# Optimization experiments

Measured on AMD Instinct MI355X. Metric: run time of the kernel, lower is better.

## Reference

```python
import jax, jax.numpy as jnp
import numpy as np

B, S, H = 2, 1024, 1024
NH, HD = 16, 64
W = 4  # attention_window / number of cached previous-layer states
LS_INIT = 0.1  # layer_scale_init_value
EPS = 1e-5


def _layernorm(x, scale, bias):
    mu = jnp.mean(x, axis=-1, keepdims=True)
    var = jnp.mean(jnp.square(x - mu), axis=-1, keepdims=True)
    return (x - mu) * jax.lax.rsqrt(var + EPS) * scale + bias


def _rope(x, pos):
    # x: [B, L, NH, HD], pos: [L]
    half = x.shape[-1] // 2
    freq = 1.0 / (10000.0 ** (jnp.arange(half, dtype=x.dtype) / half))
    ang = pos.astype(x.dtype)[:, None] * freq[None, :]           # [L, half]
    cos = jnp.cos(ang)[None, :, None, :]
    sin = jnp.sin(ang)[None, :, None, :]
    x1, x2 = jnp.split(x, 2, axis=-1)
    return jnp.concatenate([x1 * cos - x2 * sin, x1 * sin + x2 * cos], axis=-1)


def setup_inputs() -> dict:
    key = jax.random.key(0)
    ks = jax.random.split(key, 8)
    w_std = 0.02
    return {
        'hidden_states': jax.random.normal(ks[0], (B, S, H), jnp.float32),
        'cache_states': jax.random.normal(ks[1], (W, B, S, H), jnp.float32),
        'ln_scale': jnp.ones((H,), jnp.float32),
        'ln_bias': jnp.zeros((H,), jnp.float32),
        'Wq': jax.random.normal(ks[2], (H, NH * HD), jnp.float32) * w_std,
        'Wk': jax.random.normal(ks[3], (H, NH * HD), jnp.float32) * w_std,
        'Wv': jax.random.normal(ks[4], (H, NH * HD), jnp.float32) * w_std,
        'Wo': jax.random.normal(ks[5], (NH * HD, H), jnp.float32) * w_std,
        'gate_param': jax.random.normal(ks[6], (H,), jnp.float32),
        'layer_scale_param': jnp.full((H,), LS_INIT, jnp.float32),
    }


def reference(hidden_states, cache_states, ln_scale, ln_bias, Wq, Wk, Wv, Wo,
              gate_param, layer_scale_param):
    b, s, h = hidden_states.shape
    w = cache_states.shape[0]

    # pre-norm
    normed = _layernorm(hidden_states, ln_scale, ln_bias)

    # gather cached previous-layer states (already normalized in cache) and
    # stack them with the current layer along the KV axis: [B, (W+1)*S, H]
    prev_flat = jnp.transpose(cache_states, (1, 0, 2, 3)).reshape(b, w * s, h)
    kv_in = jnp.concatenate([prev_flat, normed], axis=1)

    q = (normed @ Wq).reshape(b, s, NH, HD)
    k = (kv_in @ Wk).reshape(b, (w + 1) * s, NH, HD)
    v = (kv_in @ Wv).reshape(b, (w + 1) * s, NH, HD)

    pos_q = jnp.arange(s)
    pos_k = jnp.tile(jnp.arange(s), w + 1)  # same token positions per layer
    q = _rope(q, pos_q)
    k = _rope(k, pos_k)

    scale = 1.0 / jnp.sqrt(jnp.asarray(HD, hidden_states.dtype))
    scores = jnp.einsum('bqhd,bkhd->bhqk', q, k) * scale   # [B,NH,S,(W+1)S]
    attn = jax.nn.softmax(scores, axis=-1)
    ctx = jnp.einsum('bhqk,bkhd->bqhd', attn, v).reshape(b, s, NH * HD)
    attn_out = ctx @ Wo

    # gated residual with layer scale; cross_layer = most recent cached state
    cross_layer = cache_states[-1]
    g = jax.nn.sigmoid(gate_param)
    combined = g * attn_out + (1.0 - g) * cross_layer
    output = hidden_states + layer_scale_param * combined

    # LRU cache update: evict oldest slot, append normalized new state
    new_state = _layernorm(output, ln_scale, ln_bias)
    new_cache = jnp.concatenate([cache_states[1:], new_state[None]], axis=0)
    return output, new_cache
```

## Files before the change

### kernel.cpp

```cpp
#include <hip/hip_runtime.h>
#include <math.h>

typedef unsigned short u16;

constexpr int cB = 2;
constexpr int cS = 1024;
constexpr int cH = 1024;
constexpr int cNH = 16;
constexpr int cHD = 64;
constexpr int cW = 4;
constexpr int cL = (cW + 1) * cS;
constexpr float cEPS = 1e-5f;

typedef short s16x8 __attribute__((ext_vector_type(8)));
typedef float f32x4 __attribute__((ext_vector_type(4)));

__device__ __forceinline__ float u2f(u16 u) {
  union { unsigned int i; float f; } x; x.i = ((unsigned int)u) << 16; return x.f;
}
__device__ __forceinline__ u16 f2u(float f) {
  union { float f; unsigned int i; } x; x.f = f;
  unsigned int i = x.i;
  i += 0x7fffu + ((i >> 16) & 1u);
  return (u16)(i >> 16);
}
__device__ __forceinline__ u16 f2u_rt(float f) {
  union { __bf16 b; u16 u; } c; c.b = (__bf16)f; return c.u;
}
__device__ __forceinline__ s16x8 ld_frag(const u16* p) {
  uint4 v = *(const uint4*)p;
  union { uint4 u; s16x8 s; } c; c.u = v; return c.s;
}
__device__ __forceinline__ s16x8 u4_frag(uint4 v) {
  union { uint4 u; s16x8 s; } c; c.u = v; return c.s;
}
__device__ __forceinline__ void gl_lds16(const u16* g, u16* l) {
  __builtin_amdgcn_global_load_lds(
      (const __attribute__((address_space(1))) unsigned int*)g,
      (__attribute__((address_space(3))) unsigned int*)l, 16, 0, 0);
}
template <int CTRL>
__device__ __forceinline__ float dpp_fmax(float x) {
  union { float f; int i; } a, r;
  a.f = x;
  r.i = __builtin_amdgcn_update_dpp(a.i, a.i, CTRL, 0xF, 0xF, true);
  return fmaxf(x, r.f);
}

__global__ __launch_bounds__(256) void ln_f32(
    const float* __restrict__ src, float* __restrict__ dst,
    const float* __restrict__ scale, const float* __restrict__ bias)
{
  int r = blockIdx.x;
  int t = threadIdx.x;
  const float* sp = src + (size_t)r * cH;
  float4 x = ((const float4*)sp)[t];
  float s1 = x.x + x.y + x.z + x.w;
  float s2 = x.x * x.x + x.y * x.y + x.z * x.z + x.w * x.w;
  #pragma unroll
  for (int off = 32; off > 0; off >>= 1) {
    s1 += __shfl_down(s1, off);
    s2 += __shfl_down(s2, off);
  }
  __shared__ float w1[4], w2[4];
  __shared__ float stat[2];
  int wid = t >> 6, lid = t & 63;
  if (lid == 0) { w1[wid] = s1; w2[wid] = s2; }
  __syncthreads();
  if (t == 0) {
    float a = w1[0] + w1[1] + w1[2] + w1[3];
    float b = w2[0] + w2[1] + w2[2] + w2[3];
    float mu = a * (1.f / cH);
    float var = b * (1.f / cH) - mu * mu;
    if (var < 0.f) var = 0.f;
    stat[0] = mu; stat[1] = rsqrtf(var + cEPS);
  }
  __syncthreads();
  float mu = stat[0], rs = stat[1];
  int h0 = t * 4;
  float4 sc = *(const float4*)(scale + h0);
  float4 bi = *(const float4*)(bias + h0);
  float4 o;
  o.x = (x.x - mu) * rs * sc.x + bi.x;
  o.y = (x.y - mu) * rs * sc.y + bi.y;
  o.z = (x.z - mu) * rs * sc.z + bi.z;
  o.w = (x.w - mu) * rs * sc.w + bi.w;
  *(float4*)(dst + (size_t)r * cH + h0) = o;
}

__global__ __launch_bounds__(256) void prep(
    const float* __restrict__ W0, const float* __restrict__ W1,
    const float* __restrict__ W2, const float* __restrict__ W3,
    u16* __restrict__ Wt,
    const float* __restrict__ cache, u16* __restrict__ kvin,
    const float* __restrict__ hidden,
    const float* __restrict__ scale, const float* __restrict__ bias)
{
  __shared__ float tile[32][33];
  __shared__ float red[10];
  int t = threadIdx.x;
  int bid = blockIdx.x;
  if (bid < 4096) {
    int mat = bid >> 10;
    int k0 = ((bid >> 5) & 31) * 32, n0 = (bid & 31) * 32;
    const float* W = (mat == 0) ? W0 : (mat == 1) ? W1 : (mat == 2) ? W2 : W3;
    u16* out = Wt + (size_t)mat * cH * cH;
    int r = t >> 3, c = (t & 7) * 4;
    float4 v = *(const float4*)(W + (size_t)(k0 + r) * cH + n0 + c);
    tile[r][c] = v.x; tile[r][c + 1] = v.y; tile[r][c + 2] = v.z; tile[r][c + 3] = v.w;
    __syncthreads();
    ushort4 o; u16* op = (u16*)&o;
    #pragma unroll
    for (int j = 0; j < 4; j++) op[j] = f2u(tile[c + j][r]);
    *(ushort4*)(out + (size_t)(n0 + r) * cH + k0 + c) = o;
  } else if (bid < 12288) {
    int blk = bid - 4096;
    int b = blk >> 12, w = (blk >> 10) & 3, s = blk & 1023;
    const float* src = cache + ((size_t)((w * cB + b) * cS + s)) * cH;
    u16* dst = kvin + ((size_t)(b * cL + w * cS + s)) * cH;
    float4 v = *(const float4*)(src + t * 4);
    ushort4 o; u16* op = (u16*)&o;
    op[0] = f2u(v.x); op[1] = f2u(v.y); op[2] = f2u(v.z); op[3] = f2u(v.w);
    *(ushort4*)(dst + t * 4) = o;
  } else {
    int r = bid - 12288;
    const float* sp = hidden + (size_t)r * cH;
    float4 x = ((const float4*)sp)[t];
    float s1 = x.x + x.y + x.z + x.w;
    float s2 = x.x * x.x + x.y * x.y + x.z * x.z + x.w * x.w;
    #pragma unroll
    for (int off = 32; off > 0; off >>= 1) {
      s1 += __shfl_down(s1, off);
      s2 += __shfl_down(s2, off);
    }
    int wid = t >> 6, lid = t & 63;
    if (lid == 0) { red[wid] = s1; red[4 + wid] = s2; }
    __syncthreads();
    if (t == 0) {
      float a = red[0] + red[1] + red[2] + red[3];
      float b2 = red[4] + red[5] + red[6] + red[7];
      float mu = a * (1.f / cH);
      float var = b2 * (1.f / cH) - mu * mu;
      if (var < 0.f) var = 0.f;
      red[8] = mu; red[9] = rsqrtf(var + cEPS);
    }
    __syncthreads();
    float mu = red[8], rs = red[9];
    int h0 = t * 4;
    float4 sc = *(const float4*)(scale + h0);
    float4 bi = *(const float4*)(bias + h0);
    int b = r >> 10, s = r & (cS - 1);
    u16* dp = kvin + ((size_t)(b * cL + cW * cS + s)) * cH + h0;
    ushort4 o; u16* op = (u16*)&o;
    op[0] = f2u((x.x - mu) * rs * sc.x + bi.x);
    op[1] = f2u((x.y - mu) * rs * sc.y + bi.y);
    op[2] = f2u((x.z - mu) * rs * sc.z + bi.z);
    op[3] = f2u((x.w - mu) * rs * sc.w + bi.w);
    *(ushort4*)dp = o;
  }
}

constexpr int GBM = 128, GBN = 128, TLD = 136;

__global__ __launch_bounds__(256) void mgemm(
    const u16* __restrict__ A, const u16* __restrict__ Wt,
    int a_rpb, int a_base, int a_stride,
    int c_rpb, int mode,
    u16* __restrict__ Cb, u16* __restrict__ Cb2,
    const float* __restrict__ hidden, const float* __restrict__ cachefull,
    const float* __restrict__ gate, const float* __restrict__ lsc,
    float* __restrict__ outp)
{
  __shared__ __align__(16) u16 smem[128 * TLD];

  int t = threadIdx.x;
  int m0 = blockIdx.y * GBM, n0 = blockIdx.x * GBN;
  int wave = t >> 6, lane = t & 63, l15 = lane & 15, quad = lane >> 4;
  int wm = (wave >> 1) * 64, wn = (wave & 1) * 64;

  int sr = t >> 2, sk = (t & 3) * 8;
  int rg0 = m0 + sr, rg1 = rg0 + 64;
  int ab0 = rg0 / a_rpb, ab1 = rg1 / a_rpb;
  const u16* arow0 = A + (size_t)(ab0 * a_stride + a_base + (rg0 - ab0 * a_rpb)) * cH + sk;
  const u16* arow1 = A + (size_t)(ab1 * a_stride + a_base + (rg1 - ab1 * a_rpb)) * cH + sk;
  const u16* wrow0 = Wt + (size_t)(n0 + sr) * cH + sk;
  const u16* wrow1 = Wt + (size_t)(n0 + sr + 64) * cH + sk;

  u16* As0 = smem;
  u16* Bs0 = smem + 8192;
  int wofs = wave * 512;

  f32x4 acc[4][4] = {};

  gl_lds16(arow0, As0 + wofs);
  gl_lds16(arow1, As0 + 2048 + wofs);
  gl_lds16(wrow0, Bs0 + wofs);
  gl_lds16(wrow1, Bs0 + 2048 + wofs);

  constexpr int NK = cH / 32;
  for (int kt = 0; kt < NK; kt++) {
    int cur = kt & 1;
    asm volatile("" ::: "memory");
    __builtin_amdgcn_s_barrier();
    asm volatile("" ::: "memory");
    int nk = kt + 1; if (nk == NK) nk = 0;
    int nko = nk * 32;
    u16* Abn = As0 + (cur ^ 1) * 4096;
    u16* Bbn = Bs0 + (cur ^ 1) * 4096;
    gl_lds16(arow0 + nko, Abn + wofs);
    gl_lds16(arow1 + nko, Abn + 2048 + wofs);
    gl_lds16(wrow0 + nko, Bbn + wofs);
    gl_lds16(wrow1 + nko, Bbn + 2048 + wofs);
    asm volatile("s_waitcnt vmcnt(4)" ::: "memory");
    __builtin_amdgcn_s_barrier();
    asm volatile("" ::: "memory");
    const u16* Ab = As0 + cur * 4096;
    const u16* Bb = Bs0 + cur * 4096;
    s16x8 af[4], bf[4];
    #pragma unroll
    for (int mt = 0; mt < 4; mt++)
      af[mt] = *(const s16x8*)&Ab[(wm + mt * 16 + l15) * 32 + quad * 8];
    #pragma unroll
    for (int nt = 0; nt < 4; nt++)
      bf[nt] = *(const s16x8*)&Bb[(wn + nt * 16 + l15) * 32 + quad * 8];
    #pragma unroll
    for (int mt = 0; mt < 4; mt++)
      #pragma unroll
      for (int nt = 0; nt < 4; nt++)
        acc[mt][nt] = __builtin_amdgcn_mfma_f32_16x16x32_bf16(af[mt], bf[nt], acc[mt][nt], 0, 0, 0);
  }

  int mode_eff = mode;
  u16* Cout = Cb;
  int nbase = n0;
  if (mode == 5) {
    if (n0 < cH) { mode_eff = 1; }
    else { mode_eff = 3; Cout = Cb2; nbase = n0 - cH; }
  }

  if (mode_eff == 1) {
    constexpr float RC = 13.287712379549449f / 32.f;
    float fr0 = exp2f(-(float)l15 * RC);
    float fr1 = exp2f(-(float)(l15 + 16) * RC);
    #pragma unroll
    for (int mt = 0; mt < 4; mt++)
      #pragma unroll
      for (int i = 0; i < 4; i++) {
        int rg = m0 + wm + mt * 16 + quad * 4 + i;
        int bo = rg / c_rpb, lo = rg - bo * c_rpb;
        int pos = lo & (cS - 1);
        float sn0, cs0, sn1, cs1;
        sincosf((float)pos * fr0, &sn0, &cs0);
        sincosf((float)pos * fr1, &sn1, &cs1);
        float v0 = acc[mt][0][i], v1 = acc[mt][1][i];
        float v2 = acc[mt][2][i], v3 = acc[mt][3][i];
        float rr[4];
        rr[0] = v0 * cs0 - v2 * sn0;
        rr[1] = v1 * cs1 - v3 * sn1;
        rr[2] = v0 * sn0 + v2 * cs0;
        rr[3] = v1 * sn1 + v3 * cs1;
        #pragma unroll
        for (int nt = 0; nt < 4; nt++) {
          int n = nbase + wn + nt * 16 + l15;
          int h = n >> 6, d = n & 63;
          Cout[(((size_t)(bo * cNH + h) * c_rpb + lo) * cHD) + d] = f2u(rr[nt]);
        }
      }
  } else if (mode_eff == 3) {
    u16* t2 = smem;
    asm volatile("s_waitcnt vmcnt(0)" ::: "memory");
    __syncthreads();
    #pragma unroll
    for (int mt = 0; mt < 4; mt++)
      #pragma unroll
      for (int nt = 0; nt < 4; nt++) {
        ushort4 o; u16* op = (u16*)&o;
        #pragma unroll
        for (int i = 0; i < 4; i++) op[i] = f2u(acc[mt][nt][i]);
        *(ushort4*)&t2[(size_t)(wn + nt * 16 + l15) * TLD + wm + mt * 16 + quad * 4] = o;
      }
    __syncthreads();
    int n_l = t >> 1, mh = (t & 1) * 64;
    int bo = m0 / c_rpb;
    int lo = m0 - bo * c_rpb + mh;
    int n = nbase + n_l, h = n >> 6, d = n & 63;
    u16* dst = Cout + ((size_t)(bo * cNH + h) * cHD + d) * (size_t)c_rpb + lo;
    #pragma unroll
    for (int j = 0; j < 8; j++)
      *(uint4*)(dst + j * 8) = *(const uint4*)&t2[(size_t)n_l * TLD + mh + j * 8];
  } else {
    float gv[4], lv[4];
    #pragma unroll
    for (int nt = 0; nt < 4; nt++) {
      int n = n0 + wn + nt * 16 + l15;
      gv[nt] = 1.f / (1.f + __expf(-gate[n]));
      lv[nt] = lsc[n];
    }
    #pragma unroll
    for (int mt = 0; mt < 4; mt++)
      #pragma unroll
      for (int i = 0; i < 4; i++) {
        int rg = m0 + wm + mt * 16 + quad * 4 + i;
        size_t rbase = (size_t)rg * cH;
        #pragma unroll
        for (int nt = 0; nt < 4; nt++) {
          int n = n0 + wn + nt * 16 + l15;
          float hid = hidden[rbase + n];
          float cr = cachefull[(size_t)3 * cB * cS * cH + rbase + n];
          outp[rbase + n] = hid + lv[nt] * (gv[nt] * acc[mt][nt][i] + (1.f - gv[nt]) * cr);
        }
      }
  }
}

constexpr int ACK = 64;
constexpr int PLD = 72;
constexpr int KSPLIT = 3;
constexpr int SPLT_T = 27;
constexpr int NRB = cB * cNH * cS;

__global__ __launch_bounds__(256, 3) void attn_mfma(
    const u16* __restrict__ Q, const u16* __restrict__ K, const u16* __restrict__ Vt,
    float* __restrict__ o0, float* __restrict__ o1, float* __restrict__ o2,
    float* __restrict__ mlbuf)
{
  __shared__ __align__(16) u16 kls[2][ACK * cHD];
  __shared__ u16 pbuf[4][2][16 * PLD];

  int t = threadIdx.x;
  int wave = t >> 6, lane = t & 63;
  int l15 = lane & 15, quad = lane >> 4;
  int qt = blockIdx.x, h = blockIdx.y;
  int bz = blockIdx.z;
  int b = bz & (cB - 1), split = bz >> 1;
  int q0a = qt * 128 + wave * 16;
  int q0b = q0a + 64;
  int kbase = split * SPLT_T * ACK;
  int NIT = (split == KSPLIT - 1) ? (cL / ACK - (KSPLIT - 1) * SPLT_T) : SPLT_T;

  const u16* qpa = Q + ((size_t)(b * cNH + h) * cS + q0a) * cHD;
  const u16* qpb = qpa + (size_t)64 * cHD;
  const char* kp = (const char*)(K + ((size_t)(b * cNH + h) * cL + kbase) * cHD);
  const u16* vp = Vt + (size_t)(b * cNH + h) * cHD * cL + kbase;
  u16* pwA = &pbuf[wave][0][0];
  u16* pwB = &pbuf[wave][1][0];

  int P0 = wave * 1024 + lane * 16;
  int P1 = P0 + 4096;
  int s0 = P0 ^ (((P0 >> 7) & 7) << 4);
  int s1 = P1 ^ (((P1 >> 7) & 7) << 4);
  int fsw0 = (quad * 16) ^ ((l15 & 7) << 4);
  int fsw1 = (64 + quad * 16) ^ ((l15 & 7) << 4);

  s16x8 qa0 = ld_frag(qpa + (size_t)l15 * cHD + quad * 8);
  s16x8 qa1 = ld_frag(qpa + (size_t)l15 * cHD + 32 + quad * 8);
  s16x8 qb0f = ld_frag(qpb + (size_t)l15 * cHD + quad * 8);
  s16x8 qb1f = ld_frag(qpb + (size_t)l15 * cHD + 32 + quad * 8);

  gl_lds16((const u16*)(kp + s0), (u16*)((char*)&kls[0][0] + wave * 1024));
  gl_lds16((const u16*)(kp + s1), (u16*)((char*)&kls[0][0] + 4096 + wave * 1024));

  f32x4 oacc[2][4] = {};
  float mrowA[4], lrowA[4], mrowB[4], lrowB[4];
  #pragma unroll
  for (int i = 0; i < 4; i++) {
    mrowA[i] = -1e30f; lrowA[i] = 0.f;
    mrowB[i] = -1e30f; lrowB[i] = 0.f;
  }

  constexpr float SCL = 0.125f * 1.4426950408889634f;

  for (int kt = 0; kt < NIT; kt++) {
    int cur = kt & 1;
    uint4 v01[4];
    #pragma unroll
    for (int dt = 0; dt < 2; dt++) {
      const u16* vr = vp + (size_t)(dt * 16 + l15) * cL + kt * ACK;
      v01[2 * dt]     = *(const uint4*)(vr + quad * 8);
      v01[2 * dt + 1] = *(const uint4*)(vr + 32 + quad * 8);
    }
    asm volatile("" ::: "memory");
    __builtin_amdgcn_s_barrier();
    asm volatile("" ::: "memory");
    int nk = kt + 1; if (nk == NIT) nk = 0;
    const char* kn = kp + (size_t)nk * (ACK * cHD * 2);
    gl_lds16((const u16*)(kn + s0), (u16*)((char*)&kls[cur ^ 1][0] + wave * 1024));
    gl_lds16((const u16*)(kn + s1), (u16*)((char*)&kls[cur ^ 1][0] + 4096 + wave * 1024));
    asm volatile("s_waitcnt vmcnt(6)" ::: "memory");
    __builtin_amdgcn_s_barrier();
    asm volatile("" ::: "memory");
    const char* kc = (const char*)&kls[cur][0];
    f32x4 scA[4], scB[4];
    __builtin_amdgcn_s_setprio(1);
    #pragma unroll
    for (int nt = 0; nt < 4; nt++) {
      s16x8 kf0 = *(const s16x8*)(kc + (nt * 16 + l15) * 128 + fsw0);
      s16x8 kf1 = *(const s16x8*)(kc + (nt * 16 + l15) * 128 + fsw1);
      f32x4 a = {};
      a = __builtin_amdgcn_mfma_f32_16x16x32_bf16(qa0, kf0, a, 0, 0, 0);
      a = __builtin_amdgcn_mfma_f32_16x16x32_bf16(qa1, kf1, a, 0, 0, 0);
      scA[nt] = a * SCL;
      f32x4 c = {};
      c = __builtin_amdgcn_mfma_f32_16x16x32_bf16(qb0f, kf0, c, 0, 0, 0);
      c = __builtin_amdgcn_mfma_f32_16x16x32_bf16(qb1f, kf1, c, 0, 0, 0);
      scB[nt] = c * SCL;
    }
    __builtin_amdgcn_s_setprio(0);
    float mxA[4], mxB[4];
    #pragma unroll
    for (int i = 0; i < 4; i++) {
      mxA[i] = fmaxf(fmaxf(scA[0][i], scA[1][i]), fmaxf(scA[2][i], scA[3][i]));
      mxB[i] = fmaxf(fmaxf(scB[0][i], scB[1][i]), fmaxf(scB[2][i], scB[3][i]));
    }
    #pragma unroll
    for (int i = 0; i < 4; i++) {
      mxA[i] = dpp_fmax<0xB1>(mxA[i]);  mxB[i] = dpp_fmax<0xB1>(mxB[i]);
      mxA[i] = dpp_fmax<0x4E>(mxA[i]);  mxB[i] = dpp_fmax<0x4E>(mxB[i]);
      mxA[i] = dpp_fmax<0x141>(mxA[i]); mxB[i] = dpp_fmax<0x141>(mxB[i]);
      mxA[i] = dpp_fmax<0x140>(mxA[i]); mxB[i] = dpp_fmax<0x140>(mxB[i]);
    }
    bool needA = (mxA[0] > mrowA[0]) | (mxA[1] > mrowA[1]) |
                 (mxA[2] > mrowA[2]) | (mxA[3] > mrowA[3]);
    if (__any(needA)) {
      float alpha[4];
      #pragma unroll
      for (int i = 0; i < 4; i++) {
        float mn = fmaxf(mrowA[i], mxA[i]);
        alpha[i] = exp2f(mrowA[i] - mn);
        mrowA[i] = mn;
        lrowA[i] *= alpha[i];
      }
      #pragma unroll
      for (int dt = 0; dt < 4; dt++)
        #pragma unroll
        for (int i = 0; i < 4; i++) oacc[0][dt][i] *= alpha[i];
    }
    bool needB = (mxB[0] > mrowB[0]) | (mxB[1] > mrowB[1]) |
                 (mxB[2] > mrowB[2]) | (mxB[3] > mrowB[3]);
    if (__any(needB)) {
      float alpha[4];
      #pragma unroll
      for (int i = 0; i < 4; i++) {
        float mn = fmaxf(mrowB[i], mxB[i]);
        alpha[i] = exp2f(mrowB[i] - mn);
        mrowB[i] = mn;
        lrowB[i] *= alpha[i];
      }
      #pragma unroll
      for (int dt = 0; dt < 4; dt++)
        #pragma unroll
        for (int i = 0; i < 4; i++) oacc[1][dt][i] *= alpha[i];
    }
    {
      float ps[4] = {};
      #pragma unroll
      for (int nt = 0; nt < 4; nt++)
        #pragma unroll
        for (int i = 0; i < 4; i++) {
          float p = exp2f(scA[nt][i] - mrowA[i]);
          ps[i] += p;
          pwA[(quad * 4 + i) * PLD + nt * 16 + l15] = f2u_rt(p);
        }
      #pragma unroll
      for (int i = 0; i < 4; i++) lrowA[i] += ps[i];
    }
    uint4 v23[4];
    #pragma unroll
    for (int dt = 2; dt < 4; dt++) {
      const u16* vr = vp + (size_t)(dt * 16 + l15) * cL + kt * ACK;
      v23[2 * (dt - 2)]     = *(const uint4*)(vr + quad * 8);
      v23[2 * (dt - 2) + 1] = *(const uint4*)(vr + 32 + quad * 8);
    }
    {
      float ps[4] = {};
      #pragma unroll
      for (int nt = 0; nt < 4; nt++)
        #pragma unroll
        for (int i = 0; i < 4; i++) {
          float p = exp2f(scB[nt][i] - mrowB[i]);
          ps[i] += p;
          pwB[(quad * 4 + i) * PLD + nt * 16 + l15] = f2u_rt(p);
        }
      #pragma unroll
      for (int i = 0; i < 4; i++) lrowB[i] += ps[i];
    }
    s16x8 pfA0 = *(const s16x8*)&pwA[l15 * PLD + quad * 8];
    s16x8 pfA1 = *(const s16x8*)&pwA[l15 * PLD + 32 + quad * 8];
    s16x8 pfB0 = *(const s16x8*)&pwB[l15 * PLD + quad * 8];
    s16x8 pfB1 = *(const s16x8*)&pwB[l15 * PLD + 32 + quad * 8];
    __builtin_amdgcn_s_setprio(1);
    #pragma unroll
    for (int dt = 0; dt < 2; dt++) {
      oacc[0][dt] = __builtin_amdgcn_mfma_f32_16x16x32_bf16(pfA0, u4_frag(v01[2 * dt]), oacc[0][dt], 0, 0, 0);
      oacc[0][dt] = __builtin_amdgcn_mfma_f32_16x16x32_bf16(pfA1, u4_frag(v01[2 * dt + 1]), oacc[0][dt], 0, 0, 0);
      oacc[1][dt] = __builtin_amdgcn_mfma_f32_16x16x32_bf16(pfB0, u4_frag(v01[2 * dt]), oacc[1][dt], 0, 0, 0);
      oacc[1][dt] = __builtin_amdgcn_mfma_f32_16x16x32_bf16(pfB1, u4_frag(v01[2 * dt + 1]), oacc[1][dt], 0, 0, 0);
    }
    #pragma unroll
    for (int dt = 2; dt < 4; dt++) {
      int vi = 2 * (dt - 2);
      oacc[0][dt] = __builtin_amdgcn_mfma_f32_16x16x32_bf16(pfA0, u4_frag(v23[vi]), oacc[0][dt], 0, 0, 0);
      oacc[0][dt] = __builtin_amdgcn_mfma_f32_16x16x32_bf16(pfA1, u4_frag(v23[vi + 1]), oacc[0][dt], 0, 0, 0);
      oacc[1][dt] = __builtin_amdgcn_mfma_f32_16x16x32_bf16(pfB0, u4_frag(v23[vi]), oacc[1][dt], 0, 0, 0);
      oacc[1][dt] = __builtin_amdgcn_mfma_f32_16x16x32_bf16(pfB1, u4_frag(v23[vi + 1]), oacc[1][dt], 0, 0, 0);
    }
    __builtin_amdgcn_s_setprio(0);
  }
  #pragma unroll
  for (int off = 1; off < 16; off <<= 1)
    #pragma unroll
    for (int i = 0; i < 4; i++) {
      lrowA[i] += __shfl_xor(lrowA[i], off);
      lrowB[i] += __shfl_xor(lrowB[i], off);
    }
  float* ob = (split == 0) ? o0 : (split == 1) ? o1 : o2;
  #pragma unroll
  for (int x = 0; x < 2; x++) {
    int qbase = x ? q0b : q0a;
    #pragma unroll
    for (int i = 0; i < 4; i++) {
      int q = qbase + quad * 4 + i;
      size_t Rl = (size_t)(b * cNH + h) * cS + q;
      float* orow = ob + Rl * cHD;
      #pragma unroll
      for (int dt = 0; dt < 4; dt++)
        orow[dt * 16 + l15] = oacc[x][dt][i];
      if (l15 == 0) {
        mlbuf[((size_t)split * NRB + Rl) * 2]     = x ? mrowB[i] : mrowA[i];
        mlbuf[((size_t)split * NRB + Rl) * 2 + 1] = x ? lrowB[i] : lrowA[i];
      }
    }
  }
}

__global__ __launch_bounds__(256) void attn_merge(
    const float* __restrict__ o0, const float* __restrict__ o1,
    const float* __restrict__ o2,
    const float* __restrict__ mlbuf, u16* __restrict__ ctx)
{
  int t = threadIdx.x;
  int R = blockIdx.x * 4 + (t >> 6);
  int d = t & 63;
  float ms[KSPLIT], ls[KSPLIT];
  float m = -1e30f;
  #pragma unroll
  for (int s = 0; s < KSPLIT; s++) {
    ms[s] = mlbuf[((size_t)s * NRB + R) * 2];
    ls[s] = mlbuf[((size_t)s * NRB + R) * 2 + 1];
    m = fmaxf(m, ms[s]);
  }
  const float* ops[KSPLIT] = {o0, o1, o2};
  float num = 0.f, den = 0.f;
  #pragma unroll
  for (int s = 0; s < KSPLIT; s++) {
    float a = exp2f(ms[s] - m);
    num += ops[s][(size_t)R * cHD + d] * a;
    den += ls[s] * a;
  }
  float val = num / den;
  int q = R & (cS - 1), h = (R >> 10) & 15, b = R >> 14;
  ctx[((size_t)b * cS + q) * cH + h * cHD + d] = f2u(val);
}

extern "C" void kernel_launch(void* const* d_in, const int* in_sizes, int n_in,
                              void* d_out, int out_size, void* d_ws, size_t ws_size,
                              hipStream_t stream)
{
  const float* hidden = (const float*)d_in[0];
  const float* cache  = (const float*)d_in[1];
  const float* ln_s   = (const float*)d_in[2];
  const float* ln_b   = (const float*)d_in[3];
  const float* Wq     = (const float*)d_in[4];
  const float* Wk     = (const float*)d_in[5];
  const float* Wv     = (const float*)d_in[6];
  const float* Wo     = (const float*)d_in[7];
  const float* gate   = (const float*)d_in[8];
  const float* lsc    = (const float*)d_in[9];
  float* outp = (float*)d_out;

  u16* kvin = (u16*)d_ws;
  u16* vt   = kvin + (size_t)cB * cL * cH;
  float* opart = (float*)(vt + (size_t)cB * cL * cH);
  float* o0 = opart;
  float* o1 = opart + (size_t)cB * cNH * cS * cHD;
  u16* qb  = kvin;
  u16* ctx = kvin + (size_t)2 * 1024 * 1024;
  float* o2 = (float*)(kvin + (size_t)4 * 1024 * 1024);
  float* mlbuf = (float*)(kvin + (size_t)8 * 1024 * 1024);
  u16* kb = (u16*)(outp + (size_t)cB * cS * cH);
  u16* Wt = (u16*)(outp + (size_t)(1 + 3) * cB * cS * cH);
  u16* Wt_q = Wt;
  u16* Wt_k = Wt + (size_t)cH * cH;
  u16* Wt_o = Wt + (size_t)3 * cH * cH;

  prep<<<14336, 256, 0, stream>>>(Wq, Wk, Wv, Wo, Wt, cache, kvin,
                                  hidden, ln_s, ln_b);

  mgemm<<<dim3(16, (cB * cL) / GBM), 256, 0, stream>>>(
      kvin, Wt_k, cL, 0, cL, cL, 5, kb, vt, nullptr, nullptr, nullptr, nullptr, nullptr);
  mgemm<<<dim3(8, (cB * cS) / GBM), 256, 0, stream>>>(
      kvin, Wt_q, cS, cW * cS, cL, cS, 1, qb, nullptr, nullptr, nullptr, nullptr, nullptr, nullptr);

  attn_mfma<<<dim3(cS / 128, cNH, cB * KSPLIT), 256, 0, stream>>>(
      qb, kb, vt, o0, o1, o2, mlbuf);
  attn_merge<<<(cB * cNH * cS) / 4, 256, 0, stream>>>(o0, o1, o2, mlbuf, ctx);

  mgemm<<<dim3(8, (cB * cS) / GBM), 256, 0, stream>>>(
      ctx, Wt_o, cB * cS, 0, cB * cS, cB * cS, 2, nullptr, nullptr,
      hidden, cache, gate, lsc, outp);

  hipMemcpyAsync(outp + (size_t)cB * cS * cH, cache + (size_t)cB * cS * cH,
                 (size_t)(cW - 1) * cB * cS * cH * sizeof(float),
                 hipMemcpyDeviceToDevice, stream);
  ln_f32<<<cB * cS, 256, 0, stream>>>(outp, outp + (size_t)cW * cB * cS * cH, ln_s, ln_b);
}
```

Measured before the change: 365.8 us.

## Merge Q and KV projection GEMMs into one launch; precompute RoPE table

```diff
diff --git a/kernel.cpp b/kernel.cpp
--- a/kernel.cpp
+++ b/kernel.cpp
@@ -94,7 +94,8 @@
     u16* __restrict__ Wt,
     const float* __restrict__ cache, u16* __restrict__ kvin,
     const float* __restrict__ hidden,
-    const float* __restrict__ scale, const float* __restrict__ bias)
+    const float* __restrict__ scale, const float* __restrict__ bias,
+    float2* __restrict__ ropetab)
 {
   __shared__ float tile[32][33];
   __shared__ float red[10];
@@ -122,7 +123,7 @@
     ushort4 o; u16* op = (u16*)&o;
     op[0] = f2u(v.x); op[1] = f2u(v.y); op[2] = f2u(v.z); op[3] = f2u(v.w);
     *(ushort4*)(dst + t * 4) = o;
-  } else {
+  } else if (bid < 14336) {
     int r = bid - 12288;
     const float* sp = hidden + (size_t)r * cH;
     float4 x = ((const float4*)sp)[t];
@@ -157,6 +158,14 @@
     op[2] = f2u((x.z - mu) * rs * sc.z + bi.z);
     op[3] = f2u((x.w - mu) * rs * sc.w + bi.w);
     *(ushort4*)dp = o;
+  } else {
+    int idx = (bid - 14336) * 256 + t;
+    int pos = idx >> 5, d = idx & 31;
+    constexpr float RC = 13.287712379549449f / 32.f;
+    float fr = exp2f(-(float)d * RC);
+    float sn, cs;
+    sincosf((float)pos * fr, &sn, &cs);
+    ropetab[idx] = make_float2(cs, sn);
   }
 }
 
@@ -166,7 +175,8 @@
     const u16* __restrict__ A, const u16* __restrict__ Wt,
     int a_rpb, int a_base, int a_stride,
     int c_rpb, int mode,
-    u16* __restrict__ Cb, u16* __restrict__ Cb2,
+    u16* __restrict__ Cb, u16* __restrict__ Cb2, u16* __restrict__ Cb3,
+    const float2* __restrict__ ropetab,
     const float* __restrict__ hidden, const float* __restrict__ cachefull,
     const float* __restrict__ gate, const float* __restrict__ lsc,
     float* __restrict__ outp)
@@ -174,7 +184,27 @@
   __shared__ __align__(16) u16 smem[128 * TLD];
 
   int t = threadIdx.x;
-  int m0 = blockIdx.y * GBM, n0 = blockIdx.x * GBN;
+  int bx = blockIdx.x, by = blockIdx.y;
+  int eff_mode = mode;
+  const u16* WtU = Wt;
+  u16* CbU = Cb; u16* Cb2U = Cb2;
+  if (mode == 6) {
+    if (bx < 1280) {
+      eff_mode = 5;
+      by = bx >> 4; bx = bx & 15;
+      a_rpb = cL; a_base = 0; a_stride = cL; c_rpb = cL;
+      WtU = Wt + (size_t)cH * cH;
+    } else {
+      eff_mode = 1;
+      int id = bx - 1280;
+      by = id >> 3; bx = id & 7;
+      a_rpb = cS; a_base = cW * cS; a_stride = cL; c_rpb = cS;
+      WtU = Wt;
+      CbU = Cb3;
+    }
+  }
+
+  int m0 = by * GBM, n0 = bx * GBN;
   int wave = t >> 6, lane = t & 63, l15 = lane & 15, quad = lane >> 4;
   int wm = (wave >> 1) * 64, wn = (wave & 1) * 64;
 
@@ -183,8 +213,8 @@
   int ab0 = rg0 / a_rpb, ab1 = rg1 / a_rpb;
   const u16* arow0 = A + (size_t)(ab0 * a_stride + a_base + (rg0 - ab0 * a_rpb)) * cH + sk;
   const u16* arow1 = A + (size_t)(ab1 * a_stride + a_base + (rg1 - ab1 * a_rpb)) * cH + sk;
-  const u16* wrow0 = Wt + (size_t)(n0 + sr) * cH + sk;
-  const u16* wrow1 = Wt + (size_t)(n0 + sr + 64) * cH + sk;
+  const u16* wrow0 = WtU + (size_t)(n0 + sr) * cH + sk;
+  const u16* wrow1 = WtU + (size_t)(n0 + sr + 64) * cH + sk;
 
   u16* As0 = smem;
   u16* Bs0 = smem + 8192;
@@ -230,18 +260,15 @@
         acc[mt][nt] = __builtin_amdgcn_mfma_f32_16x16x32_bf16(af[mt], bf[nt], acc[mt][nt], 0, 0, 0);
   }
 
-  int mode_eff = mode;
-  u16* Cout = Cb;
+  int mode_eff = eff_mode;
+  u16* Cout = CbU;
   int nbase = n0;
-  if (mode == 5) {
+  if (eff_mode == 5) {
     if (n0 < cH) { mode_eff = 1; }
-    else { mode_eff = 3; Cout = Cb2; nbase = n0 - cH; }
+    else { mode_eff = 3; Cout = Cb2U; nbase = n0 - cH; }
   }
 
   if (mode_eff == 1) {
-    constexpr float RC = 13.287712379549449f / 32.f;
-    float fr0 = exp2f(-(float)l15 * RC);
-    float fr1 = exp2f(-(float)(l15 + 16) * RC);
     #pragma unroll
     for (int mt = 0; mt < 4; mt++)
       #pragma unroll
@@ -249,16 +276,16 @@
         int rg = m0 + wm + mt * 16 + quad * 4 + i;
         int bo = rg / c_rpb, lo = rg - bo * c_rpb;
         int pos = lo & (cS - 1);
-        float sn0, cs0, sn1, cs1;
-        sincosf((float)pos * fr0, &sn0, &cs0);
-        sincosf((float)pos * fr1, &sn1, &cs1);
+        const float2* tb = ropetab + (size_t)pos * 32;
+        float2 c0 = tb[l15];
+        float2 c1 = tb[l15 + 16];
         float v0 = acc[mt][0][i], v1 = acc[mt][1][i];
         float v2 = acc[mt][2][i], v3 = acc[mt][3][i];
         float rr[4];
-        rr[0] = v0 * cs0 - v2 * sn0;
-        rr[1] = v1 * cs1 - v3 * sn1;
-        rr[2] = v0 * sn0 + v2 * cs0;
-        rr[3] = v1 * sn1 + v3 * cs1;
+        rr[0] = v0 * c0.x - v2 * c0.y;
+        rr[1] = v1 * c1.x - v3 * c1.y;
+        rr[2] = v0 * c0.y + v2 * c0.x;
+        rr[3] = v1 * c1.y + v3 * c1.x;
         #pragma unroll
         for (int nt = 0; nt < 4; nt++) {
           int n = nbase + wn + nt * 16 + l15;
@@ -583,31 +610,29 @@
   float* opart = (float*)(vt + (size_t)cB * cL * cH);
   float* o0 = opart;
   float* o1 = opart + (size_t)cB * cNH * cS * cHD;
-  u16* qb  = kvin;
+  float2* ropetab = (float2*)(o1 + (size_t)cB * cNH * cS * cHD);
   u16* ctx = kvin + (size_t)2 * 1024 * 1024;
   float* o2 = (float*)(kvin + (size_t)4 * 1024 * 1024);
   float* mlbuf = (float*)(kvin + (size_t)8 * 1024 * 1024);
   u16* kb = (u16*)(outp + (size_t)cB * cS * cH);
+  u16* qb = (u16*)(outp + (size_t)7 * cB * cS * cH / 2);
   u16* Wt = (u16*)(outp + (size_t)(1 + 3) * cB * cS * cH);
-  u16* Wt_q = Wt;
-  u16* Wt_k = Wt + (size_t)cH * cH;
   u16* Wt_o = Wt + (size_t)3 * cH * cH;
 
-  prep<<<14336, 256, 0, stream>>>(Wq, Wk, Wv, Wo, Wt, cache, kvin,
-                                  hidden, ln_s, ln_b);
-
-  mgemm<<<dim3(16, (cB * cL) / GBM), 256, 0, stream>>>(
-      kvin, Wt_k, cL, 0, cL, cL, 5, kb, vt, nullptr, nullptr, nullptr, nullptr, nullptr);
-  mgemm<<<dim3(8, (cB * cS) / GBM), 256, 0, stream>>>(
-      kvin, Wt_q, cS, cW * cS, cL, cS, 1, qb, nullptr, nullptr, nullptr, nullptr, nullptr, nullptr);
+  prep<<<14464, 256, 0, stream>>>(Wq, Wk, Wv, Wo, Wt, cache, kvin,
+                                  hidden, ln_s, ln_b, ropetab);
+
+  mgemm<<<1408, 256, 0, stream>>>(
+      kvin, Wt, 0, 0, 0, 0, 6, kb, vt, qb, (const float2*)ropetab,
+      nullptr, nullptr, nullptr, nullptr, nullptr);
 
   attn_mfma<<<dim3(cS / 128, cNH, cB * KSPLIT), 256, 0, stream>>>(
       qb, kb, vt, o0, o1, o2, mlbuf);
   attn_merge<<<(cB * cNH * cS) / 4, 256, 0, stream>>>(o0, o1, o2, mlbuf, ctx);
 
   mgemm<<<dim3(8, (cB * cS) / GBM), 256, 0, stream>>>(
-      ctx, Wt_o, cB * cS, 0, cB * cS, cB * cS, 2, nullptr, nullptr,
-      hidden, cache, gate, lsc, outp);
+      ctx, Wt_o, cB * cS, 0, cB * cS, cB * cS, 2, nullptr, nullptr, nullptr,
+      nullptr, hidden, cache, gate, lsc, outp);
 
   hipMemcpyAsync(outp + (size_t)cB * cS * cH, cache + (size_t)cB * cS * cH,
                  (size_t)(cW - 1) * cB * cS * cH * sizeof(float),
```

Result: faster. 352.6 us (-3.6%).
